# Performance work log

Hardware: AMD Instinct MI355X
Metric: run time of the kernel (lower is better)

## Reference

```python
import jax, jax.numpy as jnp
import numpy as np

N_STEP = 3
N_INP = 256


def setup_inputs() -> dict:
    key = jax.random.key(0)
    ks = jax.random.split(key, 8)
    bs, L, n = 16, 128, N_INP
    s = 1.0 / np.sqrt(n)
    s2 = 1.0 / np.sqrt(2 * n)
    feat = jax.random.normal(ks[0], (bs, L, n), dtype=jnp.float32)
    mask = jnp.ones((bs, L), dtype=jnp.float32)
    # stacked per-step Linear params (torch Linear: y = x @ W.T + b)
    aggW = jax.random.uniform(ks[1], (N_STEP, n, n), minval=-s, maxval=s, dtype=jnp.float32)
    aggB = jax.random.uniform(ks[2], (N_STEP, n), minval=-s, maxval=s, dtype=jnp.float32)
    attnW = jax.random.uniform(ks[3], (N_STEP, n, 2 * n), minval=-s2, maxval=s2, dtype=jnp.float32)
    attnB = jax.random.uniform(ks[4], (N_STEP, n), minval=-s2, maxval=s2, dtype=jnp.float32)
    updW = jax.random.uniform(ks[5], (N_STEP, n, 2 * n), minval=-s2, maxval=s2, dtype=jnp.float32)
    updB = jax.random.uniform(ks[6], (N_STEP, n), minval=-s2, maxval=s2, dtype=jnp.float32)
    return {"feat": feat, "mask": mask, "aggW": aggW, "aggB": aggB,
            "attnW": attnW, "attnB": attnB, "updW": updW, "updB": updB}


def reference(feat, mask, aggW, aggB, attnW, attnB, updW, updB):
    bs, L, n = feat.shape
    hid = feat
    for i in range(N_STEP):
        hid = hid * mask[:, :, None]
        x = hid @ aggW[i].T + aggB[i]  # [b, s, n]
        # attn Linear on concat(x_s, x_j) splits into two matmuls
        W1 = attnW[i][:, :n]   # acts on x_s (sequence position)
        W2 = attnW[i][:, n:]   # acts on x_j (query node)
        p = x @ W1.T           # [b, s, n]
        q = x @ W2.T           # [b, j, n]
        # logits[b, j, s, c] = p[b, s, c] + q[b, j, c] + bias[c]
        logits = p[:, None, :, :] + q[:, :, None, :] + attnB[i]
        w = jax.nn.softmax(logits, axis=2)  # softmax over sequence dim per channel
        agg = jax.nn.sigmoid(jnp.einsum('bjsn,bsn->bjn', w, x))
        cat = jnp.concatenate([x, agg], axis=-1)  # [b, s, 2n]; dropout is identity (eval)
        hid = cat @ updW[i].T + updB[i]
    return hid
```

## Files before the change

kernel.cpp:

```cpp
#include <hip/hip_runtime.h>
#include <hip/hip_fp16.h>

#define NBLK  256
#define NPACK 192
#define NT    512
#define FPAD  16

typedef _Float16 h2_t  __attribute__((ext_vector_type(2)));
typedef _Float16 half8 __attribute__((ext_vector_type(8)));
typedef float    f32x4 __attribute__((ext_vector_type(4)));

#define AG_LD(p)    __hip_atomic_load((p), __ATOMIC_RELAXED, __HIP_MEMORY_SCOPE_AGENT)
#define AG_ST(p, v) __hip_atomic_store((p), (v), __ATOMIC_RELAXED, __HIP_MEMORY_SCOPE_AGENT)

__device__ __forceinline__ unsigned pkh(float a, float b) {
    const __half2 h = __floats2half2_rn(a, b);
    return __builtin_bit_cast(unsigned, h);
}
__device__ __forceinline__ float fdot2(unsigned w, unsigned a, float c) {
#if __has_builtin(__builtin_amdgcn_fdot2)
    return __builtin_amdgcn_fdot2(__builtin_bit_cast(h2_t, w),
                                  __builtin_bit_cast(h2_t, a), c, false);
#else
    const float2 fw = __half22float2(__builtin_bit_cast(__half2, w));
    const float2 fa = __half22float2(__builtin_bit_cast(__half2, a));
    return c + fw.x * fa.x + fw.y * fa.y;
#endif
}

__device__ __forceinline__ half8 ldw(const unsigned* p) {
    return __builtin_bit_cast(half8, *(const uint4*)p);
}
__device__ __forceinline__ f32x4 MF(half8 a, half8 b, f32x4 c) {
    return __builtin_amdgcn_mfma_f32_16x16x32_f16(a, b, c, 0, 0, 0);
}

__device__ __forceinline__ void bar_arrive(int n, unsigned* flags, int lid) {
    __syncthreads();
    if (threadIdx.x == 0)
        __hip_atomic_store(&flags[lid * FPAD], (unsigned)n, __ATOMIC_RELEASE,
                           __HIP_MEMORY_SCOPE_AGENT);
}
__device__ __forceinline__ void bar_wait_batch(int n, unsigned* flags, int b) {
    if (threadIdx.x < 16) {
        while ((int)__hip_atomic_load(&flags[(b * 16 + threadIdx.x) * FPAD],
                                      __ATOMIC_RELAXED,
                                      __HIP_MEMORY_SCOPE_AGENT) < n)
            __builtin_amdgcn_s_sleep(1);
    }
    __syncthreads();
}


__global__ __launch_bounds__(NT, 2) void pack_k(
    const float* __restrict__ aggW, const float* __restrict__ attnW,
    const float* __restrict__ updW, unsigned* __restrict__ WtH,
    unsigned* __restrict__ flags)
{
    __shared__ float Tl[64][65];
    const int bb = blockIdx.x, tid = threadIdx.x;
    const int m = bb >> 4, t = bb & 15, tr = t >> 2, tc = t & 3;
    const float* src; int stride, off;
    if (m < 3)      { src = aggW  + (size_t)m * 65536;        stride = 256; off = 0;   }
    else if (m < 6) { src = attnW + (size_t)(m - 3) * 131072; stride = 512; off = 0;   }
    else if (m < 9) { src = updW  + (size_t)(m - 6) * 131072; stride = 512; off = 0;   }
    else            { src = updW  + (size_t)(m - 9) * 131072; stride = 512; off = 256; }
    unsigned* dstu = WtH + (size_t)m * 32768;
    #pragma unroll
    for (int it = 0; it < 2; ++it) {
        const int j = it * 512 + tid, row = j >> 4, q = (j & 15) * 4;
        const float4 v = *(const float4*)(src + (size_t)(tr * 64 + row) * stride + off + tc * 64 + q);
        Tl[row][q + 0] = v.x; Tl[row][q + 1] = v.y;
        Tl[row][q + 2] = v.z; Tl[row][q + 3] = v.w;
    }
    if (bb == 0)
        for (int z = tid; z < NBLK * FPAD; z += NT) flags[z] = 0u;
    __syncthreads();
    #pragma unroll
    for (int it = 0; it < 4; ++it) {
        const int j = it * 512 + tid, cl = j >> 5, pr = j & 31;
        const unsigned val = pkh(Tl[cl][pr * 2], Tl[cl][pr * 2 + 1]);
        const int C = tr * 64 + cl, P = tc * 32 + pr;
        size_t idx;
        if (m < 9) {
            const int ttn = C >> 4, lc = C & 15;
            const int kc = P >> 4, g = (P >> 2) & 3, sl = P & 3;
            idx = (size_t)((ttn * 8 + kc) * 256 + (g * 16 + lc) * 4 + sl);
        } else {
            idx = (size_t)(P >> 2) * 1024 + (size_t)C * 4 + (P & 3);
        }
        dstu[idx] = val;
    }
}

__device__ __forceinline__ float phaseB(int i, int b, int c, int rq, int tid,
                                        const float* __restrict__ part,
                                        const unsigned* __restrict__ WtH,
                                        const float* __restrict__ updB,
                                        float* S, float* aggl32, unsigned* aggh) {
    const float* pbase = part + (size_t)((i & 1) * 256 + b * 16 + rq * 8) * 768;
    float m[8], d[8], nn[8];
    #pragma unroll
    for (int j = 0; j < 8; ++j) {
        const float* pp = pbase + (size_t)j * 768;
        m[j]  = AG_LD(pp + c);
        d[j]  = AG_LD(pp + 256 + c);
        nn[j] = AG_LD(pp + 512 + c);
    }
    #pragma unroll
    for (int st = 1; st < 8; st <<= 1) {
        #pragma unroll
        for (int j = 0; j < 8; j += 2 * st) {
            const float Mn = fmaxf(m[j], m[j + st]);
            const float sa = __expf(m[j] - Mn), sb = __expf(m[j + st] - Mn);
            d[j]  = d[j] * sa + d[j + st] * sb;
            nn[j] = nn[j] * sa + nn[j + st] * sb;
            m[j]  = Mn;
        }
    }
    S[rq * 256 + c] = m[0];
    S[512 + rq * 256 + c] = d[0];
    S[1024 + rq * 256 + c] = nn[0];
    __syncthreads();
    if (rq == 0) {
        const float m0 = S[c], m1 = S[256 + c];
        const float Mx = fmaxf(m0, m1);
        const float s0 = __expf(m0 - Mx), s1 = __expf(m1 - Mx);
        const float dd = S[512 + c] * s0 + S[768 + c] * s1;
        const float nv = S[1024 + c] * s0 + S[1280 + c] * s1;
        aggl32[c] = 1.f / (1.f + __expf(-(nv / dd)));
    }
    __syncthreads();
    if (tid < 128) aggh[tid] = pkh(aggl32[2 * tid], aggl32[2 * tid + 1]);
    __syncthreads();
    const unsigned* Uq = WtH + (size_t)(9 + i) * 32768;
    const int g0 = rq * 16;
    uint4 buf[8];
    #pragma unroll
    for (int j = 0; j < 8; ++j)
        buf[j] = *(const uint4*)(Uq + (size_t)(g0 + j) * 1024 + c * 4);
    float au = 0.f;
    #pragma unroll
    for (int ph = 0; ph < 2; ++ph) {
        #pragma unroll
        for (int j = 0; j < 8; ++j) {
            const uint4 w = buf[j];
            if (ph < 1)
                buf[j] = *(const uint4*)(Uq + (size_t)(g0 + 8 + j) * 1024 + c * 4);
            const uint4 a = *(const uint4*)&aggh[(g0 + ph * 8 + j) * 4];
            au = fdot2(w.x, a.x, au);
            au = fdot2(w.y, a.y, au);
            au = fdot2(w.z, a.z, au);
            au = fdot2(w.w, a.w, au);
        }
    }
    __syncthreads();
    S[rq * 256 + c] = au;
    __syncthreads();
    return S[c] + S[256 + c] + updB[i * 256 + c];
}

__global__ __launch_bounds__(NT, 2) void main_k(
    const float* __restrict__ feat,
    const float* __restrict__ mask,
    const float* __restrict__ aggB,
    const float* __restrict__ updB,
    const unsigned* __restrict__ WtH,
    float* __restrict__ part,
    unsigned* flags,
    float* __restrict__ out)
{
    __shared__ __align__(16) float ldsf[6408];
    unsigned* hid_uu = (unsigned*)ldsf;
    unsigned* x_uu   = (unsigned*)ldsf + 2112;
    float*    accl   = ldsf + 4224;
    float*    S      = ldsf + 4480;
    float*    aggl32 = ldsf + 6016;
    unsigned* aggh   = (unsigned*)ldsf + 6272;
    float*    msk    = ldsf + 6400;

    const int bid = blockIdx.x;
    const int tid = threadIdx.x;
    const int c   = tid & 255;
    const int rq  = tid >> 8;
    const int wid = tid >> 6, lane = tid & 63;
    const int lr  = lane & 15, lg = lane >> 4;
    const int b   = 2 * (bid & 7) + ((bid >> 3) & 1);
    const int jj  = bid >> 4;
    const int lid = b * 16 + jj;
    const int row0 = b * 128 + jj * 8;

    #pragma unroll
    for (int it = 0; it < 2; ++it) {
        const int j = it * 512 + tid, r = j >> 7, pr = j & 127;
        const float2 f = *(const float2*)(feat + (size_t)(row0 + r) * 256 + pr * 2);
        const float mv = mask[row0 + r];
        hid_uu[r * 132 + pr] = pkh(f.x * mv, f.y * mv);
    }
    for (int z = tid; z < 1056; z += NT) hid_uu[1056 + z] = 0u;
    for (int z = tid; z < 1056; z += NT) x_uu[1056 + z] = 0u;
    if (tid < 8) msk[tid] = mask[row0 + tid];
    __syncthreads();

    f32x4 xu0 = {}, xu1 = {};

    for (int i = 0; i < 3; ++i) {
        if (i > 0) {
            const float accU = phaseB(i - 1, b, c, rq, tid, part, WtH, updB,
                                      S, aggl32, aggh);
            if (rq == 0) accl[c] = accU;
            __syncthreads();
            #pragma unroll
            for (int tt = 0; tt < 2; ++tt) {
                const int t = wid * 2 + tt;
                const f32x4 xa = tt ? xu1 : xu0;
                const float av = accl[t * 16 + lr];
                float hv[4], pv[4];
                #pragma unroll
                for (int q = 0; q < 4; ++q)
                    hv[q] = (xa[q] + av) * msk[(lg & 1) * 4 + q];
                #pragma unroll
                for (int q = 0; q < 4; ++q) pv[q] = __shfl_xor(hv[q], 1);
                if (lg < 2 && !(lr & 1)) {
                    const int p2 = t * 8 + (lr >> 1);
                    #pragma unroll
                    for (int q = 0; q < 4; ++q)
                        hid_uu[(lg * 4 + q) * 132 + p2] = pkh(hv[q], pv[q]);
                }
            }
            __syncthreads();
        }

        f32x4 xr0, xr1;

        {
            const unsigned* W0 = WtH + (size_t)i * 32768;
            half8 a[8];
            #pragma unroll
            for (int kc = 0; kc < 8; ++kc)
                a[kc] = ldw(hid_uu + lr * 132 + kc * 16 + lg * 4);
            #pragma unroll
            for (int tt = 0; tt < 2; ++tt) {
                const int t = wid * 2 + tt;
                f32x4 acc = {};
                #pragma unroll
                for (int kc = 0; kc < 8; ++kc)
                    acc = MF(a[kc], ldw(W0 + (size_t)(t * 8 + kc) * 256 + lane * 4), acc);
                const float bb = aggB[i * 256 + t * 16 + lr];
                #pragma unroll
                for (int q = 0; q < 4; ++q) acc[q] += bb;
                if (tt) xr1 = acc; else xr0 = acc;
                float pv[4];
                #pragma unroll
                for (int q = 0; q < 4; ++q) pv[q] = __shfl_xor(acc[q], 1);
                if (lg < 2 && !(lr & 1)) {
                    const int p2 = t * 8 + (lr >> 1);
                    #pragma unroll
                    for (int q = 0; q < 4; ++q)
                        x_uu[(lg * 4 + q) * 132 + p2] = pkh(acc[q], pv[q]);
                }
            }
            __syncthreads();
        }

        {
            const unsigned* W1 = WtH + (size_t)(3 + i) * 32768;
            const unsigned* U1 = WtH + (size_t)(6 + i) * 32768;
            half8 a2[8];
            #pragma unroll
            for (int kc = 0; kc < 8; ++kc)
                a2[kc] = ldw(x_uu + lr * 132 + kc * 16 + lg * 4);
            float* pb = part + (size_t)((i & 1) * 256 + lid) * 768;
            #pragma unroll
            for (int tt = 0; tt < 2; ++tt) {
                const int t = wid * 2 + tt;
                f32x4 acc = {};
                #pragma unroll
                for (int kc = 0; kc < 8; ++kc)
                    acc = MF(a2[kc], ldw(W1 + (size_t)(t * 8 + kc) * 256 + lane * 4), acc);
                const f32x4 xa = tt ? xr1 : xr0;
                float m4 = fmaxf(fmaxf(acc[0], acc[1]), fmaxf(acc[2], acc[3]));
                const float m8 = fmaxf(m4, __shfl_xor(m4, 16));
                float d4 = 0.f, n4 = 0.f;
                #pragma unroll
                for (int q = 0; q < 4; ++q) {
                    const float e = __expf(acc[q] - m8);
                    d4 += e;
                    n4 += e * xa[q];
                }
                const float d8 = d4 + __shfl_xor(d4, 16);
                const float n8 = n4 + __shfl_xor(n4, 16);
                if (lg == 0) {
                    const int cc = t * 16 + lr;
                    AG_ST(pb + cc, m8);
                    AG_ST(pb + 256 + cc, d8);
                    AG_ST(pb + 512 + cc, n8);
                }
            }
            bar_arrive(i + 1, flags, lid);
            #pragma unroll
            for (int tt = 0; tt < 2; ++tt) {
                const int t = wid * 2 + tt;
                f32x4 acc = {};
                #pragma unroll
                for (int kc = 0; kc < 8; ++kc)
                    acc = MF(a2[kc], ldw(U1 + (size_t)(t * 8 + kc) * 256 + lane * 4), acc);
                if (tt) xu1 = acc; else xu0 = acc;
            }
            bar_wait_batch(i + 1, flags, b);
        }
    }

    {
        const float accU = phaseB(2, b, c, rq, tid, part, WtH, updB, S, aggl32, aggh);
        if (rq == 0) accl[c] = accU;
        __syncthreads();
        #pragma unroll
        for (int tt = 0; tt < 2; ++tt) {
            const int t = wid * 2 + tt;
            const f32x4 xa = tt ? xu1 : xu0;
            const float av = accl[t * 16 + lr];
            if (lg < 2) {
                #pragma unroll
                for (int q = 0; q < 4; ++q)
                    out[(size_t)(row0 + lg * 4 + q) * 256 + t * 16 + lr] = xa[q] + av;
            }
        }
    }
}

extern "C" void kernel_launch(void* const* d_in, const int* in_sizes, int n_in,
                              void* d_out, int out_size, void* d_ws, size_t ws_size,
                              hipStream_t stream) {
    const float* feat  = (const float*)d_in[0];
    const float* mask  = (const float*)d_in[1];
    const float* aggW  = (const float*)d_in[2];
    const float* aggB  = (const float*)d_in[3];
    const float* attnW = (const float*)d_in[4];
    const float* updW  = (const float*)d_in[6];
    const float* updB  = (const float*)d_in[7];

    unsigned* WtH = (unsigned*)d_ws;
    float* part = (float*)(WtH + 12 * 32768);
    unsigned* flags = (unsigned*)(part + 2 * 256 * 768);

    pack_k<<<NPACK, NT, 0, stream>>>(aggW, attnW, updW, WtH, flags);
    main_k<<<NBLK, NT, 0, stream>>>(feat, mask, aggB, updB, WtH, part, flags,
                                    (float*)d_out);
}
```

Baseline: 109.4 us.

## Prefetch update weights before grid barrier and trim phase-B syncs

The first half of the update-weight slice used in phase B is now loaded into registers before the cross-block barrier wait, so its latency overlaps the wait instead of following it. The sigmoid/softmax merge is folded into the 128 threads that pack the half2 aggregate, which removes one LDS buffer and one __syncthreads, and a redundant barrier before the partial-sum write is dropped. The dot product now uses four independent accumulators to shorten the fdot2 dependency chain. These changes add 32 VGPRs held across the barrier, which may raise register pressure at two blocks per CU.

```diff
diff --git a/kernel.cpp b/kernel.cpp
--- a/kernel.cpp
+++ b/kernel.cpp
@@ -97,7 +97,7 @@
                                         const float* __restrict__ part,
                                         const unsigned* __restrict__ WtH,
                                         const float* __restrict__ updB,
-                                        float* S, float* aggl32, unsigned* aggh) {
+                                        float* S, unsigned* aggh, uint4* buf) {
     const float* pbase = part + (size_t)((i & 1) * 256 + b * 16 + rq * 8) * 768;
     float m[8], d[8], nn[8];
     #pragma unroll
@@ -122,24 +122,24 @@
     S[512 + rq * 256 + c] = d[0];
     S[1024 + rq * 256 + c] = nn[0];
     __syncthreads();
-    if (rq == 0) {
-        const float m0 = S[c], m1 = S[256 + c];
-        const float Mx = fmaxf(m0, m1);
-        const float s0 = __expf(m0 - Mx), s1 = __expf(m1 - Mx);
-        const float dd = S[512 + c] * s0 + S[768 + c] * s1;
-        const float nv = S[1024 + c] * s0 + S[1280 + c] * s1;
-        aggl32[c] = 1.f / (1.f + __expf(-(nv / dd)));
-    }
-    __syncthreads();
-    if (tid < 128) aggh[tid] = pkh(aggl32[2 * tid], aggl32[2 * tid + 1]);
+    if (tid < 128) {
+        float sg[2];
+        #pragma unroll
+        for (int u = 0; u < 2; ++u) {
+            const int cc = 2 * tid + u;
+            const float m0 = S[cc], m1 = S[256 + cc];
+            const float Mx = fmaxf(m0, m1);
+            const float s0 = __expf(m0 - Mx), s1 = __expf(m1 - Mx);
+            const float dd = S[512 + cc] * s0 + S[768 + cc] * s1;
+            const float nv = S[1024 + cc] * s0 + S[1280 + cc] * s1;
+            sg[u] = 1.f / (1.f + __expf(-(nv / dd)));
+        }
+        aggh[tid] = pkh(sg[0], sg[1]);
+    }
     __syncthreads();
     const unsigned* Uq = WtH + (size_t)(9 + i) * 32768;
     const int g0 = rq * 16;
-    uint4 buf[8];
-    #pragma unroll
-    for (int j = 0; j < 8; ++j)
-        buf[j] = *(const uint4*)(Uq + (size_t)(g0 + j) * 1024 + c * 4);
-    float au = 0.f;
+    float a0 = 0.f, a1 = 0.f, a2 = 0.f, a3 = 0.f;
     #pragma unroll
     for (int ph = 0; ph < 2; ++ph) {
         #pragma unroll
@@ -148,13 +148,13 @@
             if (ph < 1)
                 buf[j] = *(const uint4*)(Uq + (size_t)(g0 + 8 + j) * 1024 + c * 4);
             const uint4 a = *(const uint4*)&aggh[(g0 + ph * 8 + j) * 4];
-            au = fdot2(w.x, a.x, au);
-            au = fdot2(w.y, a.y, au);
-            au = fdot2(w.z, a.z, au);
-            au = fdot2(w.w, a.w, au);
-        }
-    }
-    __syncthreads();
+            a0 = fdot2(w.x, a.x, a0);
+            a1 = fdot2(w.y, a.y, a1);
+            a2 = fdot2(w.z, a.z, a2);
+            a3 = fdot2(w.w, a.w, a3);
+        }
+    }
+    const float au = (a0 + a1) + (a2 + a3);
     S[rq * 256 + c] = au;
     __syncthreads();
     return S[c] + S[256 + c] + updB[i * 256 + c];
@@ -170,14 +170,13 @@
     unsigned* flags,
     float* __restrict__ out)
 {
-    __shared__ __align__(16) float ldsf[6408];
+    __shared__ __align__(16) float ldsf[6152];
     unsigned* hid_uu = (unsigned*)ldsf;
     unsigned* x_uu   = (unsigned*)ldsf + 2112;
     float*    accl   = ldsf + 4224;
     float*    S      = ldsf + 4480;
-    float*    aggl32 = ldsf + 6016;
-    unsigned* aggh   = (unsigned*)ldsf + 6272;
-    float*    msk    = ldsf + 6400;
+    unsigned* aggh   = (unsigned*)ldsf + 6016;
+    float*    msk    = ldsf + 6144;
 
     const int bid = blockIdx.x;
     const int tid = threadIdx.x;
@@ -197,17 +196,20 @@
         const float mv = mask[row0 + r];
         hid_uu[r * 132 + pr] = pkh(f.x * mv, f.y * mv);
     }
-    for (int z = tid; z < 1056; z += NT) hid_uu[1056 + z] = 0u;
-    for (int z = tid; z < 1056; z += NT) x_uu[1056 + z] = 0u;
+    for (int z = tid; z < 1056; z += NT) {
+        hid_uu[1056 + z] = 0u;
+        x_uu[1056 + z] = 0u;
+    }
     if (tid < 8) msk[tid] = mask[row0 + tid];
     __syncthreads();
 
     f32x4 xu0 = {}, xu1 = {};
+    uint4 u2buf[8];
 
     for (int i = 0; i < 3; ++i) {
         if (i > 0) {
             const float accU = phaseB(i - 1, b, c, rq, tid, part, WtH, updB,
-                                      S, aggl32, aggh);
+                                      S, aggh, u2buf);
             if (rq == 0) accl[c] = accU;
             __syncthreads();
             #pragma unroll
@@ -307,12 +309,18 @@
                     acc = MF(a2[kc], ldw(U1 + (size_t)(t * 8 + kc) * 256 + lane * 4), acc);
                 if (tt) xu1 = acc; else xu0 = acc;
             }
+            {
+                const unsigned* Uq = WtH + (size_t)(9 + i) * 32768;
+                #pragma unroll
+                for (int j = 0; j < 8; ++j)
+                    u2buf[j] = *(const uint4*)(Uq + (size_t)(rq * 16 + j) * 1024 + c * 4);
+            }
             bar_wait_batch(i + 1, flags, b);
         }
     }
 
     {
-        const float accU = phaseB(2, b, c, rq, tid, part, WtH, updB, S, aggl32, aggh);
+        const float accU = phaseB(2, b, c, rq, tid, part, WtH, updB, S, aggh, u2buf);
         if (rq == 0) accl[c] = accU;
         __syncthreads();
         #pragma unroll
```

After: 109.8 us. Within noise of the previous version (+0.4%).
